# Kernel optimization log

Hardware: AMD Instinct MI355X
Metric: run time of the kernel (lower is better)

## Reference

```python
import jax, jax.numpy as jnp
import numpy as np
import math

B, S, E, H, DK = 2, 2048, 1024, 16, 64  # batch, seq, embed, heads, d_k (= n_wires)

def setup_inputs() -> dict:
    key = jax.random.key(0)
    k1, k2, k3, k4, k5 = jax.random.split(key, 5)
    scale = 0.02
    return {
        "x": jax.random.normal(k1, (B, S, E), dtype=jnp.float32),
        "Wk": jax.random.normal(k2, (E, E), dtype=jnp.float32) * scale,
        "Wv": jax.random.normal(k3, (E, E), dtype=jnp.float32) * scale,
        "Wq": jax.random.normal(k4, (H, DK, E), dtype=jnp.float32) * scale,
        "theta": jax.random.normal(k5, (DK,), dtype=jnp.float32) * scale,
    }

def reference(x, Wk, Wv, Wq, theta):
    batch, seq, embed = x.shape
    n_heads, d_k = Wq.shape[0], Wq.shape[1]
    # K, V projections (nn.Linear, no bias): x @ W.T
    k = (x @ Wk.T).reshape(batch, seq, n_heads, d_k).transpose(0, 2, 1, 3)  # [B,H,S,dk]
    v = (x @ Wv.T).reshape(batch, seq, n_heads, d_k).transpose(0, 2, 1, 3)  # [B,H,S,dk]
    # Quantum query path: per-head linear proj -> RX(proj_i) then RX(theta_i) on wire i from |0>,
    # MeasureAll(PauliZ) on independent wires gives <Z_i> = cos(proj_i + theta_i) exactly.
    proj = jnp.einsum('bse,hde->bhsd', x, Wq)          # [B,H,S,dk]
    q = jnp.cos(proj + theta)                           # [B,H,S,dk]
    scores = jnp.einsum('bhsd,bhtd->bhst', q, k) / math.sqrt(d_k)  # [B,H,S,S]
    attn = jax.nn.softmax(scores, axis=-1)
    out = jnp.einsum('bhst,bhtd->bhsd', attn, v)        # [B,H,S,dk]
    return out.transpose(0, 2, 1, 3).reshape(batch, seq, embed)
```

## Files before the change

### kernel.cpp

```cpp
#include <hip/hip_runtime.h>
#include <hip/hip_bf16.h>

constexpr int B  = 2;
constexpr int S  = 2048;
constexpr int E  = 1024;
constexpr int H  = 16;
constexpr int DK = 64;
constexpr int M  = B * S;
constexpr int N3 = 3 * E;
constexpr long RSZ = (long)B * H * S * DK;

#define QSCALE 0.18033688011112042f

using bf16x8 = __attribute__((ext_vector_type(8))) __bf16;
using bf16x4 = __attribute__((ext_vector_type(4))) __bf16;
using f32x4  = __attribute__((ext_vector_type(4))) float;

__device__ __forceinline__ void async16(__bf16* lds, const __bf16* g) {
    __builtin_amdgcn_global_load_lds(
        (const __attribute__((address_space(1))) void*)g,
        (__attribute__((address_space(3))) void*)lds, 16, 0, 0);
}

__global__ __launch_bounds__(256)
void cvt_kernel(const float* __restrict__ x, const float* __restrict__ Wk,
                const float* __restrict__ Wv, const float* __restrict__ Wq,
                __bf16* __restrict__ xb, __bf16* __restrict__ wall) {
    const long e = ((long)blockIdx.x * 256 + threadIdx.x) * 4;
    const float* src;
    __bf16* dst;
    if (e < (long)M * E) { src = x + e; dst = xb + e; }
    else {
        const long e2 = e - (long)M * E;
        const int which = (int)(e2 >> 20);
        const long off  = e2 & ((1L << 20) - 1);
        src = (which == 0 ? Wk : which == 1 ? Wv : Wq) + off;
        dst = wall + e2;
    }
    float4 f = *reinterpret_cast<const float4*>(src);
    bf16x4 o;
    o[0] = (__bf16)f.x; o[1] = (__bf16)f.y; o[2] = (__bf16)f.z; o[3] = (__bf16)f.w;
    *reinterpret_cast<bf16x4*>(dst) = o;
}

__global__ __launch_bounds__(256, 3)
void qkv_gemm(const __bf16* __restrict__ xb, const __bf16* __restrict__ wall,
              const float* __restrict__ theta, __bf16* __restrict__ kvq) {
    __shared__ __align__(1024) __bf16 smem[6 * 128 * 32];
    __bf16* tile = smem;

    const int t    = threadIdx.x;
    const int lane = t & 63;
    const int w    = t >> 6;
    const int quad = lane >> 4;
    const int l16  = lane & 15;
    const int wm   = w >> 1, wn = w & 1;
    const int mbase = blockIdx.y * 128;
    const int nbase = blockIdx.x * 128;

    f32x4 acc[4][4];
    #pragma unroll
    for (int i = 0; i < 4; i++)
        #pragma unroll
        for (int j = 0; j < 4; j++)
            acc[i][j] = f32x4{0.f, 0.f, 0.f, 0.f};

    const int srow = lane >> 2;
    const int srcc = (lane & 3) ^ ((lane >> 3) & 3);
    const __bf16* ga = xb   + (long)(mbase + srow) * E + srcc * 8;
    const __bf16* gb = wall + (long)(nbase + srow) * E + srcc * 8;

    const int csw = (l16 >> 1) & 3;

    #pragma unroll
    for (int pt = 0; pt < 2; pt++) {
        #pragma unroll
        for (int c = 0; c < 2; c++) {
            async16(smem + pt * 4096 +         (c * 64 + w * 16) * 32,
                    ga + (long)(c * 64 + w * 16) * E + pt * 32);
            async16(smem + pt * 4096 + 12288 + (c * 64 + w * 16) * 32,
                    gb + (long)(c * 64 + w * 16) * E + pt * 32);
        }
    }

    int cur = 0;
    constexpr int ITERS = E / 32;
    for (int it = 0; it < ITERS; it++) {
        if (it < ITERS - 1) asm volatile("s_waitcnt vmcnt(4)" ::: "memory");
        else                asm volatile("s_waitcnt vmcnt(0)" ::: "memory");
        asm volatile("s_barrier" ::: "memory");

        if (it + 2 < ITERS) {
            const int pb  = (cur == 0) ? 2 : cur - 1;
            const int kk2 = (it + 2) * 32;
            #pragma unroll
            for (int c = 0; c < 2; c++) {
                async16(smem + pb * 4096 +         (c * 64 + w * 16) * 32,
                        ga + (long)(c * 64 + w * 16) * E + kk2);
                async16(smem + pb * 4096 + 12288 + (c * 64 + w * 16) * 32,
                        gb + (long)(c * 64 + w * 16) * E + kk2);
            }
        }

        const __bf16* Asb = smem + cur * 4096;
        const __bf16* Bsb = smem + cur * 4096 + 12288;
        bf16x8 a[4], b[4];
        #pragma unroll
        for (int i = 0; i < 4; i++)
            a[i] = *reinterpret_cast<const bf16x8*>(
                &Asb[(wm * 64 + i * 16 + l16) * 32 + (quad ^ csw) * 8]);
        #pragma unroll
        for (int j = 0; j < 4; j++)
            b[j] = *reinterpret_cast<const bf16x8*>(
                &Bsb[(wn * 64 + j * 16 + l16) * 32 + (quad ^ csw) * 8]);
        #pragma unroll
        for (int i = 0; i < 4; i++)
            #pragma unroll
            for (int j = 0; j < 4; j++)
                acc[i][j] = __builtin_amdgcn_mfma_f32_16x16x32_bf16(a[i], b[j], acc[i][j], 0, 0, 0);

        cur = (cur == 2) ? 0 : cur + 1;
    }

    const int region = nbase >> 10;
    const int bb = mbase >> 11;
    if (region == 1) {
        __syncthreads();
        #pragma unroll
        for (int i = 0; i < 4; i++) {
            const int cchunk = wm * 8 + i * 2 + (quad >> 1);
            #pragma unroll
            for (int j = 0; j < 4; j++) {
                const int cirb = wn * 64 + j * 16 + l16;
                const int cs = cchunk ^ l16;
                bf16x4 pk;
                #pragma unroll
                for (int r = 0; r < 4; r++) pk[r] = (__bf16)acc[i][j][r];
                *reinterpret_cast<bf16x4*>(&tile[cirb * 128 + cs * 8 + (quad & 1) * 4]) = pk;
            }
        }
        __syncthreads();
        const int h0 = (nbase & 1023) >> 6;
        __bf16* vt = kvq + RSZ;
        #pragma unroll
        for (int p = 0; p < 8; p++) {
            const int dcol = p * 16 + (t >> 4);
            const int lc = t & 15;
            const int cs2 = lc ^ (dcol & 15);
            bf16x8 vv = *reinterpret_cast<const bf16x8*>(&tile[dcol * 128 + cs2 * 8]);
            const int hh = h0 + (dcol >> 6), d = dcol & 63;
            *reinterpret_cast<bf16x8*>(
                &vt[((long)(bb * H + hh) * DK + d) * S + (mbase & 2047) + lc * 8]) = vv;
        }
    } else {
        __bf16* dst = kvq + (region == 2 ? 2 * RSZ : 0);
        float th[4];
        if (region == 2) {
            #pragma unroll
            for (int j = 0; j < 4; j++) th[j] = theta[j * 16 + l16];
        }
        #pragma unroll
        for (int i = 0; i < 4; i++) {
            const int row0 = mbase + wm * 64 + i * 16 + quad * 4;
            #pragma unroll
            for (int j = 0; j < 4; j++) {
                const int cir = (nbase & 1023) + wn * 64 + j * 16 + l16;
                const int h = cir >> 6, d = cir & 63;
                #pragma unroll
                for (int r = 0; r < 4; r++) {
                    const int s = (row0 + r) & 2047;
                    float v = acc[i][j][r];
                    if (region == 2) v = cosf(v + th[j]) * QSCALE;
                    dst[((long)(bb * H + h) * S + s) * DK + d] = (__bf16)v;
                }
            }
        }
    }
}

__global__ __launch_bounds__(256, 3)
void attn_kernel(const __bf16* __restrict__ q_ws, const __bf16* __restrict__ k_ws,
                 const __bf16* __restrict__ v_ws, float* __restrict__ out) {
    __shared__ __align__(1024) __bf16 Ks[2][64 * 64];
    __shared__ __align__(1024) __bf16 Vs[2][64 * 64];
    __shared__ __align__(16)   __bf16 Pl[4][16 * 72];
    __shared__ __align__(16)   float  ls_lds[4][16];

    const int lane = threadIdx.x & 63;
    const int w    = threadIdx.x >> 6;
    const int quad = lane >> 4;
    const int l16  = lane & 15;

    const int id    = blockIdx.x;
    const int bh    = (id & 7) + 8 * ((id >> 3) & 3);
    const int qbase = (id >> 5) * 64 + w * 16;

    const __bf16* qp = q_ws + (long)bh * S * DK;
    const __bf16* kp = k_ws + (long)bh * S * DK;
    const __bf16* vp = v_ws + (long)bh * DK * S;

    const int sr  = lane >> 3;
    const int scs = (lane & 7) ^ sr;

    bf16x8 bq[2];
    #pragma unroll
    for (int ks = 0; ks < 2; ks++)
        bq[ks] = *reinterpret_cast<const bf16x8*>(
            qp + (long)(qbase + l16) * DK + ks * 32 + quad * 8);

    f32x4 o[4];
    #pragma unroll
    for (int j = 0; j < 4; j++) o[j] = f32x4{0.f, 0.f, 0.f, 0.f};
    float lsum = 0.f;

    #pragma unroll
    for (int i = 0; i < 2; i++) {
        const int row = w * 16 + i * 8;
        async16(&Ks[0][row * 64], kp + (long)(row + sr) * DK + scs * 8);
        async16(&Vs[0][row * 64], vp + (long)(row + sr) * S + scs * 8);
    }

    int cur = 0;
    constexpr int ITERS = S / 64;
    for (int it = 0; it < ITERS; it++) {
        asm volatile("s_waitcnt vmcnt(0)" ::: "memory");
        asm volatile("s_barrier" ::: "memory");

        if (it + 1 < ITERS) {
            const int kt1 = (it + 1) * 64;
            #pragma unroll
            for (int i = 0; i < 2; i++) {
                const int row = w * 16 + i * 8;
                async16(&Ks[cur ^ 1][row * 64], kp + (long)(kt1 + row + sr) * DK + scs * 8);
                async16(&Vs[cur ^ 1][row * 64], vp + (long)(row + sr) * S + kt1 + scs * 8);
            }
        }

        f32x4 sacc[4];
        #pragma unroll
        for (int i = 0; i < 4; i++) sacc[i] = f32x4{0.f, 0.f, 0.f, 0.f};
        #pragma unroll
        for (int ks = 0; ks < 2; ks++) {
            #pragma unroll
            for (int mt = 0; mt < 4; mt++) {
                bf16x8 ak = *reinterpret_cast<const bf16x8*>(
                    &Ks[cur][(mt * 16 + l16) * 64 + ((ks * 4 + quad) ^ (l16 & 7)) * 8]);
                sacc[mt] = __builtin_amdgcn_mfma_f32_16x16x32_bf16(
                    ak, bq[ks], sacc[mt], 0, 0, 0);
            }
        }

        #pragma unroll
        for (int mt = 0; mt < 4; mt++) {
            float p0 = __builtin_amdgcn_exp2f(sacc[mt][0]);
            float p1 = __builtin_amdgcn_exp2f(sacc[mt][1]);
            float p2 = __builtin_amdgcn_exp2f(sacc[mt][2]);
            float p3 = __builtin_amdgcn_exp2f(sacc[mt][3]);
            lsum += (p0 + p1) + (p2 + p3);
            bf16x4 pk;
            pk[0] = (__bf16)p0; pk[1] = (__bf16)p1;
            pk[2] = (__bf16)p2; pk[3] = (__bf16)p3;
            *reinterpret_cast<bf16x4*>(
                &Pl[w][l16 * 72 + mt * 16 + quad * 4]) = pk;
        }

        #pragma unroll
        for (int kh = 0; kh < 2; kh++) {
            bf16x8 ap = *reinterpret_cast<const bf16x8*>(
                &Pl[w][l16 * 72 + kh * 32 + quad * 8]);
            #pragma unroll
            for (int nt = 0; nt < 4; nt++) {
                bf16x8 bv = *reinterpret_cast<const bf16x8*>(
                    &Vs[cur][(nt * 16 + l16) * 64 + ((kh * 4 + quad) ^ (l16 & 7)) * 8]);
                o[nt] = __builtin_amdgcn_mfma_f32_16x16x32_bf16(
                    ap, bv, o[nt], 0, 0, 0);
            }
        }

        cur ^= 1;
    }

    {
        float v = lsum;
        v += __shfl_xor(v, 16);
        v += __shfl_xor(v, 32);
        ls_lds[w][l16] = v;
    }

    const int b = bh >> 4, h = bh & 15;
    f32x4 lv = *reinterpret_cast<const f32x4*>(&ls_lds[w][quad * 4]);
    #pragma unroll
    for (int r = 0; r < 4; r++) {
        const float inv = 1.0f / lv[r];
        const int srow = qbase + quad * 4 + r;
        #pragma unroll
        for (int nt = 0; nt < 4; nt++)
            out[(long)(b * S + srow) * E + h * DK + nt * 16 + l16] = o[nt][r] * inv;
    }
}

__device__ inline bf16x8 cvt_frag(const float* __restrict__ p) {
    float4 f0 = *reinterpret_cast<const float4*>(p);
    float4 f1 = *reinterpret_cast<const float4*>(p + 4);
    bf16x8 r;
    r[0] = (__bf16)f0.x; r[1] = (__bf16)f0.y; r[2] = (__bf16)f0.z; r[3] = (__bf16)f0.w;
    r[4] = (__bf16)f1.x; r[5] = (__bf16)f1.y; r[6] = (__bf16)f1.z; r[7] = (__bf16)f1.w;
    return r;
}
template <int MODE>
__global__ __launch_bounds__(256, 2)
void proj_kernel(const float* __restrict__ x, const float* __restrict__ W,
                 const float* __restrict__ theta, __bf16* __restrict__ out) {
    const int lane = threadIdx.x & 63;
    const int w    = threadIdx.x >> 6;
    const int quad = lane >> 4;
    const int l16  = lane & 15;
    const int mbase = blockIdx.y * 128 + w * 32;
    const int nbase = blockIdx.x * 128;
    f32x4 acc[2][8];
    #pragma unroll
    for (int i = 0; i < 2; i++)
        #pragma unroll
        for (int j = 0; j < 8; j++) acc[i][j] = f32x4{0.f, 0.f, 0.f, 0.f};
    float th[4];
    if (MODE == 2) {
        #pragma unroll
        for (int j = 0; j < 4; j++) th[j] = theta[j * 16 + l16];
    }
    for (int kk = 0; kk < E; kk += 32) {
        bf16x8 a[2], b[8];
        #pragma unroll
        for (int mt = 0; mt < 2; mt++)
            a[mt] = cvt_frag(x + (long)(mbase + mt * 16 + l16) * E + kk + quad * 8);
        #pragma unroll
        for (int nt = 0; nt < 8; nt++)
            b[nt] = cvt_frag(W + (long)(nbase + nt * 16 + l16) * E + kk + quad * 8);
        #pragma unroll
        for (int mt = 0; mt < 2; mt++)
            #pragma unroll
            for (int nt = 0; nt < 8; nt++)
                acc[mt][nt] = __builtin_amdgcn_mfma_f32_16x16x32_bf16(a[mt], b[nt], acc[mt][nt], 0, 0, 0);
    }
    #pragma unroll
    for (int mt = 0; mt < 2; mt++) {
        const int row0 = mbase + mt * 16 + quad * 4;
        #pragma unroll
        for (int nt = 0; nt < 8; nt++) {
            const int col = nbase + nt * 16 + l16;
            const int h = col >> 6, d = col & 63;
            #pragma unroll
            for (int r = 0; r < 4; r++) {
                const int row = row0 + r;
                const int bb = row >> 11, s = row & 2047;
                float v = acc[mt][nt][r];
                if (MODE == 2) v = cosf(v + th[nt & 3]) * QSCALE;
                long idx;
                if (MODE == 1) idx = ((long)(bb * H + h) * DK + d) * S + s;
                else           idx = ((long)(bb * H + h) * S + s) * DK + d;
                out[idx] = (__bf16)v;
            }
        }
    }
}

extern "C" void kernel_launch(void* const* d_in, const int* in_sizes, int n_in,
                              void* d_out, int out_size, void* d_ws, size_t ws_size,
                              hipStream_t stream) {
    const float* x     = (const float*)d_in[0];
    const float* Wk    = (const float*)d_in[1];
    const float* Wv    = (const float*)d_in[2];
    const float* Wq    = (const float*)d_in[3];
    const float* theta = (const float*)d_in[4];
    float* out = (float*)d_out;

    __bf16* kvq  = (__bf16*)d_ws;
    __bf16* xb   = kvq + 3 * RSZ;
    __bf16* wall = xb + (long)M * E;
    __bf16* k_ws = kvq;
    __bf16* v_t  = kvq + RSZ;
    __bf16* q_ws = kvq + 2 * RSZ;

    const size_t need = (3 * RSZ + (long)M * E + (long)N3 * E) * 2;
    dim3 blk(256);
    if (ws_size >= need) {
        cvt_kernel<<<dim3(7168), blk, 0, stream>>>(x, Wk, Wv, Wq, xb, wall);
        qkv_gemm<<<dim3(N3 / 128, M / 128), blk, 0, stream>>>(xb, wall, theta, kvq);
    } else {
        dim3 gp(E / 128, M / 128);
        proj_kernel<0><<<gp, blk, 0, stream>>>(x, Wk, nullptr, k_ws);
        proj_kernel<1><<<gp, blk, 0, stream>>>(x, Wv, nullptr, v_t);
        proj_kernel<2><<<gp, blk, 0, stream>>>(x, Wq, theta, q_ws);
    }

    attn_kernel<<<dim3(1024), blk, 0, stream>>>(q_ws, k_ws, v_t, out);
}
```

Before: 191.8 us.

## Switch attention to 32x32 MFMA tiles with register-resident P via permlane swaps

The attention kernel moves from 16x16x32 MFMA to 32x32x16 MFMA, so each wave handles 32 query rows and each block 128, with half as many blocks. The probability tile is no longer staged through LDS. It is repacked in registers with permlane32_swap into the A-operand layout for the PV product, which removes the Pl shared buffer and its LDS round trip. Each K/V tile loaded into LDS is now reused across twice as many queries, at the cost of more registers per thread, a reduced occupancy hint (3 to 2), and only 512 blocks to spread across the CUs.

```diff
diff --git a/kernel.cpp b/kernel.cpp
--- a/kernel.cpp
+++ b/kernel.cpp
@@ -15,11 +15,19 @@
 using bf16x8 = __attribute__((ext_vector_type(8))) __bf16;
 using bf16x4 = __attribute__((ext_vector_type(4))) __bf16;
 using f32x4  = __attribute__((ext_vector_type(4))) float;
+using f32x16 = __attribute__((ext_vector_type(16))) float;
+using u32x4  = __attribute__((ext_vector_type(4))) unsigned int;
 
 __device__ __forceinline__ void async16(__bf16* lds, const __bf16* g) {
     __builtin_amdgcn_global_load_lds(
         (const __attribute__((address_space(1))) void*)g,
         (__attribute__((address_space(3))) void*)lds, 16, 0, 0);
+}
+
+__device__ __forceinline__ unsigned pack_bf16x2(float a, float b) {
+    unsigned short lo = __builtin_bit_cast(unsigned short, (__bf16)a);
+    unsigned short hi = __builtin_bit_cast(unsigned short, (__bf16)b);
+    return (unsigned)lo | ((unsigned)hi << 16);
 }
 
 __global__ __launch_bounds__(256)
@@ -178,22 +186,22 @@
     }
 }
 
-__global__ __launch_bounds__(256, 3)
+__global__ __launch_bounds__(256, 2)
 void attn_kernel(const __bf16* __restrict__ q_ws, const __bf16* __restrict__ k_ws,
                  const __bf16* __restrict__ v_ws, float* __restrict__ out) {
     __shared__ __align__(1024) __bf16 Ks[2][64 * 64];
     __shared__ __align__(1024) __bf16 Vs[2][64 * 64];
-    __shared__ __align__(16)   __bf16 Pl[4][16 * 72];
-    __shared__ __align__(16)   float  ls_lds[4][16];
+    __shared__ __align__(16)   float  ls_lds[4][32];
 
     const int lane = threadIdx.x & 63;
     const int w    = threadIdx.x >> 6;
-    const int quad = lane >> 4;
-    const int l16  = lane & 15;
+    const int l32  = lane & 31;
+    const int hi   = lane >> 5;
+    const int swz  = lane & 7;
 
     const int id    = blockIdx.x;
     const int bh    = (id & 7) + 8 * ((id >> 3) & 3);
-    const int qbase = (id >> 5) * 64 + w * 16;
+    const int qbase = (id >> 5) * 128 + w * 32;
 
     const __bf16* qp = q_ws + (long)bh * S * DK;
     const __bf16* kp = k_ws + (long)bh * S * DK;
@@ -202,15 +210,15 @@
     const int sr  = lane >> 3;
     const int scs = (lane & 7) ^ sr;
 
-    bf16x8 bq[2];
-    #pragma unroll
-    for (int ks = 0; ks < 2; ks++)
-        bq[ks] = *reinterpret_cast<const bf16x8*>(
-            qp + (long)(qbase + l16) * DK + ks * 32 + quad * 8);
-
-    f32x4 o[4];
-    #pragma unroll
-    for (int j = 0; j < 4; j++) o[j] = f32x4{0.f, 0.f, 0.f, 0.f};
+    bf16x8 bq[4];
+    #pragma unroll
+    for (int ds = 0; ds < 4; ds++)
+        bq[ds] = *reinterpret_cast<const bf16x8*>(
+            qp + (long)(qbase + l32) * DK + ds * 16 + hi * 8);
+
+    f32x16 o[2];
+    o[0] = (f32x16)0.0f;
+    o[1] = (f32x16)0.0f;
     float lsum = 0.f;
 
     #pragma unroll
@@ -236,66 +244,73 @@
             }
         }
 
-        f32x4 sacc[4];
-        #pragma unroll
-        for (int i = 0; i < 4; i++) sacc[i] = f32x4{0.f, 0.f, 0.f, 0.f};
-        #pragma unroll
-        for (int ks = 0; ks < 2; ks++) {
-            #pragma unroll
-            for (int mt = 0; mt < 4; mt++) {
+        f32x16 sacc[2];
+        sacc[0] = (f32x16)0.0f;
+        sacc[1] = (f32x16)0.0f;
+        #pragma unroll
+        for (int ds = 0; ds < 4; ds++)
+            #pragma unroll
+            for (int kb = 0; kb < 2; kb++) {
                 bf16x8 ak = *reinterpret_cast<const bf16x8*>(
-                    &Ks[cur][(mt * 16 + l16) * 64 + ((ks * 4 + quad) ^ (l16 & 7)) * 8]);
-                sacc[mt] = __builtin_amdgcn_mfma_f32_16x16x32_bf16(
-                    ak, bq[ks], sacc[mt], 0, 0, 0);
-            }
-        }
-
-        #pragma unroll
-        for (int mt = 0; mt < 4; mt++) {
-            float p0 = __builtin_amdgcn_exp2f(sacc[mt][0]);
-            float p1 = __builtin_amdgcn_exp2f(sacc[mt][1]);
-            float p2 = __builtin_amdgcn_exp2f(sacc[mt][2]);
-            float p3 = __builtin_amdgcn_exp2f(sacc[mt][3]);
-            lsum += (p0 + p1) + (p2 + p3);
-            bf16x4 pk;
-            pk[0] = (__bf16)p0; pk[1] = (__bf16)p1;
-            pk[2] = (__bf16)p2; pk[3] = (__bf16)p3;
-            *reinterpret_cast<bf16x4*>(
-                &Pl[w][l16 * 72 + mt * 16 + quad * 4]) = pk;
-        }
-
-        #pragma unroll
-        for (int kh = 0; kh < 2; kh++) {
-            bf16x8 ap = *reinterpret_cast<const bf16x8*>(
-                &Pl[w][l16 * 72 + kh * 32 + quad * 8]);
-            #pragma unroll
-            for (int nt = 0; nt < 4; nt++) {
-                bf16x8 bv = *reinterpret_cast<const bf16x8*>(
-                    &Vs[cur][(nt * 16 + l16) * 64 + ((kh * 4 + quad) ^ (l16 & 7)) * 8]);
-                o[nt] = __builtin_amdgcn_mfma_f32_16x16x32_bf16(
-                    ap, bv, o[nt], 0, 0, 0);
-            }
-        }
+                    &Ks[cur][(kb * 32 + l32) * 64 + ((ds * 2 + hi) ^ swz) * 8]);
+                sacc[kb] = __builtin_amdgcn_mfma_f32_32x32x16_bf16(
+                    ak, bq[ds], sacc[kb], 0, 0, 0);
+            }
+
+        bf16x8 ap[2][2];
+        #pragma unroll
+        for (int kb = 0; kb < 2; kb++) {
+            float p[16];
+            #pragma unroll
+            for (int r = 0; r < 16; r++) {
+                p[r] = __builtin_amdgcn_exp2f(sacc[kb][r]);
+                lsum += p[r];
+            }
+            unsigned c[8];
+            #pragma unroll
+            for (int i = 0; i < 8; i++)
+                c[i] = pack_bf16x2(p[2 * i], p[2 * i + 1]);
+            #pragma unroll
+            for (int kst = 0; kst < 2; kst++) {
+                auto s0 = __builtin_amdgcn_permlane32_swap(
+                    c[kst * 4 + 0], c[kst * 4 + 2], false, false);
+                auto s1 = __builtin_amdgcn_permlane32_swap(
+                    c[kst * 4 + 1], c[kst * 4 + 3], false, false);
+                u32x4 t;
+                t[0] = s0[0]; t[1] = s1[0]; t[2] = s0[1]; t[3] = s1[1];
+                ap[kb][kst] = __builtin_bit_cast(bf16x8, t);
+            }
+        }
+
+        #pragma unroll
+        for (int kb = 0; kb < 2; kb++)
+            #pragma unroll
+            for (int kst = 0; kst < 2; kst++) {
+                const int gk = kb * 2 + kst;
+                #pragma unroll
+                for (int nt = 0; nt < 2; nt++) {
+                    bf16x8 bv = *reinterpret_cast<const bf16x8*>(
+                        &Vs[cur][(nt * 32 + l32) * 64 + ((gk * 2 + hi) ^ swz) * 8]);
+                    o[nt] = __builtin_amdgcn_mfma_f32_32x32x16_bf16(
+                        ap[kb][kst], bv, o[nt], 0, 0, 0);
+                }
+            }
 
         cur ^= 1;
     }
 
-    {
-        float v = lsum;
-        v += __shfl_xor(v, 16);
-        v += __shfl_xor(v, 32);
-        ls_lds[w][l16] = v;
-    }
+    lsum += __shfl_xor(lsum, 32);
+    ls_lds[w][l32] = lsum;
 
     const int b = bh >> 4, h = bh & 15;
-    f32x4 lv = *reinterpret_cast<const f32x4*>(&ls_lds[w][quad * 4]);
-    #pragma unroll
-    for (int r = 0; r < 4; r++) {
-        const float inv = 1.0f / lv[r];
-        const int srow = qbase + quad * 4 + r;
-        #pragma unroll
-        for (int nt = 0; nt < 4; nt++)
-            out[(long)(b * S + srow) * E + h * DK + nt * 16 + l16] = o[nt][r] * inv;
+    #pragma unroll
+    for (int r = 0; r < 16; r++) {
+        const int qr = (r & 3) + 8 * (r >> 2) + 4 * hi;
+        const float inv = 1.0f / ls_lds[w][qr];
+        const int srow = qbase + qr;
+        #pragma unroll
+        for (int nt = 0; nt < 2; nt++)
+            out[(long)(b * S + srow) * E + h * DK + nt * 32 + l32] = o[nt][r] * inv;
     }
 }
 
@@ -392,5 +407,5 @@
         proj_kernel<2><<<gp, blk, 0, stream>>>(x, Wq, theta, q_ws);
     }
 
-    attn_kernel<<<dim3(1024), blk, 0, stream>>>(q_ws, k_ws, v_t, out);
-}
+    attn_kernel<<<dim3(512), blk, 0, stream>>>(q_ws, k_ws, v_t, out);
+}
```

After: 173.7 us. -9.4%, faster.
